# Performance work log

Hardware: AMD Instinct MI355X
Metric: run time of the kernel (lower is better)

## Reference

```python
import jax, jax.numpy as jnp
import numpy as np

DT = 1e-3   # time step (s)
DX = 10.0   # grid spacing (m)


def laplacian(u):
    # 5-point stencil with zero-Dirichlet boundaries; u: (B, ny, nx)
    up = jnp.pad(u, ((0, 0), (1, 1), (1, 1)))
    return (up[:, 2:, 1:-1] + up[:, :-2, 1:-1]
            + up[:, 1:-1, 2:] + up[:, 1:-1, :-2]
            - 4.0 * u) / (DX * DX)


def setup_inputs() -> dict:
    key = jax.random.key(0)
    ks = jax.random.split(key, 6)
    B, ny, nx, nt, R = 4, 256, 256, 300, 128
    x = jax.random.normal(ks[0], (B, nt), dtype=jnp.float32)          # source wavelets
    vp = 1500.0 + 1000.0 * jax.random.uniform(ks[1], (ny, nx), dtype=jnp.float32)
    src_y = jax.random.randint(ks[2], (B,), 2, ny - 2)
    src_x = jax.random.randint(ks[3], (B,), 2, nx - 2)
    rec_y = jax.random.randint(ks[4], (R,), 2, ny - 2)
    rec_x = jax.random.randint(ks[5], (R,), 2, nx - 2)
    return {"x": x, "vp": vp, "src_y": src_y, "src_x": src_x,
            "rec_y": rec_y, "rec_x": rec_x}


def reference(x, vp, src_y, src_x, rec_y, rec_x):
    # x: (B, nt) source amplitudes; vp: (ny, nx) velocity model.
    B = x.shape[0]
    ny, nx = vp.shape
    c2dt2 = (vp * vp) * (DT * DT)        # (ny, nx), vp^2 dt^2
    bidx = jnp.arange(B)

    def step(carry, xt):
        h1, h2 = carry                                    # u_t, u_{t-1}
        hn = 2.0 * h1 - h2 + c2dt2[None] * laplacian(h1)  # leapfrog update
        hn = hn.at[bidx, src_y, src_x].add(xt)            # source injection (scatter)
        rec = hn[:, rec_y, rec_x]                         # probe gather -> (B, R)
        return (hn, h1), rec

    h0 = jnp.zeros((B, ny, nx), dtype=x.dtype)
    _, recs = jax.lax.scan(step, (h0, h0), x.T)           # recs: (nt, B, R)
    y = jnp.transpose(recs, (0, 2, 1))                    # (nt, R, B) as in torch permute(1,2,0)
    return y
```

## Files before the change

kernel.cpp:

```cpp
#include <hip/hip_runtime.h>


constexpr int B_   = 4;
constexpr int NY   = 256;
constexpr int NX   = 256;
constexpr int NT   = 300;
constexpr int RCV  = 128;

constexpr int QB   = 16;
constexpr int RB   = NY / QB;
constexpr int W    = 8;
constexpr int EXT  = RB + 2 * W;
constexpr int GRIDB= 128;
constexpr int NTHR = 512;
constexpr int ROWS = 4;
constexpr int NW   = EXT / ROWS;
constexpr int SLABR= EXT + 2;
constexpr int PUBR = 2 * W - 1;
constexpr int LINKS= B_ * (QB - 1);
constexpr size_t HALO_FLOATS = (size_t)LINKS * 2 * 2 * PUBR * NX;
constexpr size_t HALO_BYTES  = HALO_FLOATS * sizeof(float);
constexpr int FSTR = 64;
constexpr size_t CTRL_INTS = (size_t)GRIDB * FSTR + GRIDB;
constexpr int SPIN_LIM = 1 << 20;

typedef float f32x4 __attribute__((ext_vector_type(4)));

__device__ __forceinline__ void at_store2(float* p, float a, float b) {
    float2 v = make_float2(a, b);
    unsigned long long u;
    __builtin_memcpy(&u, &v, 8);
    __hip_atomic_store((unsigned long long*)p, u, __ATOMIC_RELAXED,
                       __HIP_MEMORY_SCOPE_AGENT);
}
__device__ __forceinline__ float2 at_load2(const float* p) {
    unsigned long long u = __hip_atomic_load((const unsigned long long*)p,
                                             __ATOMIC_RELAXED,
                                             __HIP_MEMORY_SCOPE_AGENT);
    float2 v;
    __builtin_memcpy(&v, &u, 8);
    return v;
}
__device__ __forceinline__ int ld_flag_sc0(const int* p) {
    int v;
    asm volatile("global_load_dword %0, %1, off sc0\n\ts_waitcnt vmcnt(0)"
                 : "=v"(v) : "v"(p) : "memory");
    return v;
}
__device__ __forceinline__ void pub2(float* dst, const float v[4]) {
    *reinterpret_cast<float4*>(dst) = make_float4(v[0], v[1], v[2], v[3]);
    at_store2(dst, v[0], v[1]);
    at_store2(dst + 2, v[2], v[3]);
}
__device__ __forceinline__ void ing2(const float* src, float v[4], bool fast) {
    if (fast) {
        f32x4 t;
        asm volatile("global_load_dwordx4 %0, %1, off sc0\n\ts_waitcnt vmcnt(0)"
                     : "=v"(t) : "v"(src) : "memory");
        v[0] = t.x; v[1] = t.y; v[2] = t.z; v[3] = t.w;
    } else {
        float2 a = at_load2(src), b2 = at_load2(src + 2);
        v[0] = a.x; v[1] = a.y; v[2] = b2.x; v[3] = b2.y;
    }
}
__device__ __forceinline__ bool dual_wait(const int* fastp, const int* slowp,
                                          int tgt) {
    int g = 0;
    for (;;) {
        if (ld_flag_sc0(fastp) >= tgt) return true;
        if (__hip_atomic_load(slowp, __ATOMIC_RELAXED,
                              __HIP_MEMORY_SCOPE_AGENT) >= tgt) return false;
        if (++g > SPIN_LIM) return false;
        __builtin_amdgcn_s_sleep(1);
    }
}

__global__ __launch_bounds__(NTHR, 1)
void wave_df2(const float* __restrict__ x,
              const float* __restrict__ vp,
              const int*   __restrict__ src_y,
              const int*   __restrict__ src_x,
              const int*   __restrict__ rec_y,
              const int*   __restrict__ rec_x,
              float*       __restrict__ y,
              float*       __restrict__ halo,
              int*         __restrict__ ctrl)
{
    const int blk = blockIdx.x;
    const int b = blk & 7;
    if (b >= B_) return;
    const int q = blk >> 3;

    __shared__ float slabs[2][SLABR][NX];

    const int tid = threadIdx.x;
    const int r0 = q * RB;
    const int w = tid >> 6, lane = tid & 63;
    const int c0 = lane * 4;
    const int e0 = ROWS * w;

    int* fastf = ctrl;
    int* slowf = ctrl + GRIDB * FSTR;

    for (int i = tid; i < 2 * SLABR * NX; i += NTHR) ((float*)slabs)[i] = 0.f;

    const float scale = 1e-8f;
    float hA[ROWS][4], hB[ROWS][4], c2[ROWS][4];
#pragma unroll
    for (int rr = 0; rr < ROWS; ++rr) {
        const int gr = r0 - W + e0 + rr;
        if (gr >= 0 && gr < NY) {
            float4 v = *reinterpret_cast<const float4*>(&vp[gr * NX + c0]);
            c2[rr][0] = v.x * v.x * scale; c2[rr][1] = v.y * v.y * scale;
            c2[rr][2] = v.z * v.z * scale; c2[rr][3] = v.w * v.w * scale;
        } else {
#pragma unroll
            for (int j = 0; j < 4; ++j) c2[rr][j] = 0.f;
        }
#pragma unroll
        for (int j = 0; j < 4; ++j) { hA[rr][j] = 0.f; hB[rr][j] = 0.f; }
    }

    const int sy = src_y[b], sx = src_x[b];
    const int es = sy - r0 + W;
    const bool src_mine = (es >= e0) && (es < e0 + ROWS) && ((sx >> 2) == lane);
    const int s_j = sx & 3;

    bool rec_mine = false; int rec_addr = 0; float* yp = nullptr;
    if (tid < RCV) {
        const int ry = rec_y[tid], rx = rec_x[tid];
        rec_mine = (ry >= r0) && (ry < r0 + RB);
        rec_addr = (ry - r0 + W + 1) * NX + rx;
        yp = y + tid * B_ + b;
    }

    const float* xb = x + b * NT;
    const size_t lnkQ  = (size_t)(b * (QB - 1) + (q < QB - 1 ? q : 0));
    const size_t lnkQm = (size_t)(b * (QB - 1) + (q > 0 ? q - 1 : 0));
    float*       pubDn  = halo + ((lnkQ  * 2 + 0) * 2) * PUBR * NX;
    float*       pubUp  = halo + ((lnkQm * 2 + 1) * 2) * PUBR * NX;
    const float* ingTop = halo + ((lnkQm * 2 + 0) * 2) * PUBR * NX;
    const float* ingBot = halo + ((lnkQ  * 2 + 1) * 2) * PUBR * NX;

    __syncthreads();
    int exch = 0;

#define STEP(HO, HN, tt)                                                       \
    {                                                                          \
        const int cur = (tt) & 1, nxt = ((tt) + 1) & 1;                        \
        if ((tt) > 0 && rec_mine)                                              \
            yp[(size_t)((tt) - 1) * RCV * B_] =                                \
                ((const float*)slabs[cur])[rec_addr];                          \
        const float4 u4 = *reinterpret_cast<const float4*>(&slabs[cur][e0][c0]);\
        const float4 d4 = *reinterpret_cast<const float4*>(&slabs[cur][e0+ROWS+1][c0]);\
        const float ua[4] = {u4.x, u4.y, u4.z, u4.w};                          \
        const float da[4] = {d4.x, d4.y, d4.z, d4.w};                          \
        const float xt = xb[tt];                                               \
        _Pragma("unroll")                                                      \
        for (int rr = 0; rr < ROWS; ++rr) {                                    \
            float lv = __shfl_up(HO[rr][3], 1);   if (lane == 0)  lv = 0.f;    \
            float rv = __shfl_down(HO[rr][0], 1); if (lane == 63) rv = 0.f;    \
            _Pragma("unroll")                                                  \
            for (int j = 0; j < 4; ++j) {                                      \
                const float uu = (rr == 0)      ? ua[j] : HO[rr-1][j];         \
                const float dd = (rr == ROWS-1) ? da[j] : HO[rr+1][j];         \
                const float ll = (j == 0) ? lv : HO[rr][j-1];                  \
                const float rr2= (j == 3) ? rv : HO[rr][j+1];                  \
                HN[rr][j] = 2.f*HO[rr][j] - HN[rr][j]                          \
                          + c2[rr][j]*(uu + dd + ll + rr2 - 4.f*HO[rr][j]);    \
            }                                                                  \
        }                                                                      \
        if (src_mine) {                                                        \
            _Pragma("unroll")                                                  \
            for (int rr = 0; rr < ROWS; ++rr)                                  \
                _Pragma("unroll")                                              \
                for (int j = 0; j < 4; ++j)                                    \
                    if (e0 + rr == es && j == s_j) HN[rr][j] += xt;            \
        }                                                                      \
        _Pragma("unroll")                                                      \
        for (int rr = 0; rr < ROWS; ++rr)                                      \
            *reinterpret_cast<float4*>(&slabs[nxt][e0+1+rr][c0]) =             \
                make_float4(HN[rr][0], HN[rr][1], HN[rr][2], HN[rr][3]);       \
        if ((((tt) + 1) & 7) == 0) {                                           \
            ++exch;                                                            \
            const size_t soff = (size_t)(exch & 1) * PUBR * NX;                \
            _Pragma("unroll")                                                  \
            for (int rr = 0; rr < ROWS; ++rr) {                                \
                const int ext = e0 + rr;                                       \
                if (q < QB-1) {                    \
                    if (ext >= 16 && ext < 24)                                 \
                        pub2(pubDn + soff + (ext-16)*NX + c0, HN[rr]);         \
                    if (ext >= 17 && ext < 24)                                 \
                        pub2(pubDn + soff + (8+ext-17)*NX + c0, HO[rr]);       \
                }                                                              \
                if (q > 0) {                           \
                    if (ext >= 8 && ext < 16)                                  \
                        pub2(pubUp + soff + (ext-8)*NX + c0, HN[rr]);          \
                    if (ext >= 8 && ext < 15)                                  \
                        pub2(pubUp + soff + (8+ext-8)*NX + c0, HO[rr]);        \
                }                                                              \
            }                                                                  \
            __syncthreads();    \
            if (tid == 0) {                                                    \
                ((volatile int*)fastf)[blk * FSTR] = exch;        \
                __hip_atomic_store(&slowf[blk], exch, __ATOMIC_RELAXED,        \
                                   __HIP_MEMORY_SCOPE_AGENT);     \
            }                                                                  \
            if (q > 0 && w <= 1) {                   \
                const bool fast = dual_wait(&fastf[(blk-8)*FSTR],              \
                                            &slowf[blk-8], exch);              \
                _Pragma("unroll")                                              \
                for (int rr = 0; rr < ROWS; ++rr) {                            \
                    const int ext = e0 + rr;                                   \
                    if (ext < 8) {                                             \
                        ing2(ingTop + soff + ext*NX + c0, HN[rr], fast);       \
                        *reinterpret_cast<float4*>(&slabs[nxt][ext+1][c0]) =   \
                            make_float4(HN[rr][0],HN[rr][1],HN[rr][2],HN[rr][3]);\
                        if (ext >= 1)                                          \
                            ing2(ingTop + soff + (7+ext)*NX + c0, HO[rr], fast);\
                    }                                                          \
                }                                                              \
            }                                                                  \
            if (q < QB-1 && w >= NW-2) {        \
                const bool fast = dual_wait(&fastf[(blk+8)*FSTR],              \
                                            &slowf[blk+8], exch);              \
                _Pragma("unroll")                                              \
                for (int rr = 0; rr < ROWS; ++rr) {                            \
                    const int ext = e0 + rr;                                   \
                    if (ext >= 24) {                                           \
                        ing2(ingBot + soff + (ext-24)*NX + c0, HN[rr], fast);  \
                        *reinterpret_cast<float4*>(&slabs[nxt][ext+1][c0]) =   \
                            make_float4(HN[rr][0],HN[rr][1],HN[rr][2],HN[rr][3]);\
                        if (ext < 31)                                          \
                            ing2(ingBot + soff + (8+ext-24)*NX + c0, HO[rr], fast);\
                    }                                                          \
                }                                                              \
            }                                                                  \
            __syncthreads();                                                   \
        } else {                                                               \
            __syncthreads();                                                   \
        }                                                                      \
    }

    for (int t = 0; t < NT; t += 2) {
        STEP(hA, hB, t)
        STEP(hB, hA, t + 1)
    }
#undef STEP

    if (rec_mine)
        yp[(size_t)(NT - 1) * RCV * B_] = ((const float*)slabs[0])[rec_addr];
}

extern "C" void kernel_launch(void* const* d_in, const int* in_sizes, int n_in,
                              void* d_out, int out_size, void* d_ws, size_t ws_size,
                              hipStream_t stream) {
    const float* x     = (const float*)d_in[0];
    const float* vp    = (const float*)d_in[1];
    const int*   src_y = (const int*)d_in[2];
    const int*   src_x = (const int*)d_in[3];
    const int*   rec_y = (const int*)d_in[4];
    const int*   rec_x = (const int*)d_in[5];
    float*       y     = (float*)d_out;

    float* halo = (float*)d_ws;
    int*   ctrl = (int*)((char*)d_ws + HALO_BYTES);

    hipMemsetAsync(ctrl, 0, CTRL_INTS * sizeof(int), stream);

    wave_df2<<<GRIDB, NTHR, 0, stream>>>(x, vp, src_y, src_x, rec_y, rec_x,
                                         y, halo, ctrl);
}
```

Measured before the change: 371.4 us.

## Template kernel on band count, use 32 bands and LDS edge exchange

```diff
diff --git a/kernel.cpp b/kernel.cpp
--- a/kernel.cpp
+++ b/kernel.cpp
@@ -6,22 +6,11 @@
 constexpr int NX   = 256;
 constexpr int NT   = 300;
 constexpr int RCV  = 128;
-
-constexpr int QB   = 16;
-constexpr int RB   = NY / QB;
 constexpr int W    = 8;
-constexpr int EXT  = RB + 2 * W;
-constexpr int GRIDB= 128;
 constexpr int NTHR = 512;
-constexpr int ROWS = 4;
-constexpr int NW   = EXT / ROWS;
-constexpr int SLABR= EXT + 2;
 constexpr int PUBR = 2 * W - 1;
-constexpr int LINKS= B_ * (QB - 1);
-constexpr size_t HALO_FLOATS = (size_t)LINKS * 2 * 2 * PUBR * NX;
-constexpr size_t HALO_BYTES  = HALO_FLOATS * sizeof(float);
 constexpr int FSTR = 64;
-constexpr size_t CTRL_INTS = (size_t)GRIDB * FSTR + GRIDB;
+constexpr int EW   = 132;
 constexpr int SPIN_LIM = 1 << 20;
 
 typedef float f32x4 __attribute__((ext_vector_type(4)));
@@ -75,23 +64,31 @@
     }
 }
 
+template<int QB>
 __global__ __launch_bounds__(NTHR, 1)
-void wave_df2(const float* __restrict__ x,
-              const float* __restrict__ vp,
-              const int*   __restrict__ src_y,
-              const int*   __restrict__ src_x,
-              const int*   __restrict__ rec_y,
-              const int*   __restrict__ rec_x,
-              float*       __restrict__ y,
-              float*       __restrict__ halo,
-              int*         __restrict__ ctrl)
+void wave_k(const float* __restrict__ x,
+            const float* __restrict__ vp,
+            const int*   __restrict__ src_y,
+            const int*   __restrict__ src_x,
+            const int*   __restrict__ rec_y,
+            const int*   __restrict__ rec_x,
+            float*       __restrict__ y,
+            float*       __restrict__ halo,
+            int*         __restrict__ ctrl)
 {
+    constexpr int RB    = NY / QB;
+    constexpr int EXT   = RB + 2 * W;
+    constexpr int ROWS  = EXT / 8;
+    constexpr int SLABR = EXT + 2;
+    constexpr int GRIDB = 8 * QB;
+
     const int blk = blockIdx.x;
     const int b = blk & 7;
     if (b >= B_) return;
     const int q = blk >> 3;
 
     __shared__ float slabs[2][SLABR][NX];
+    __shared__ float edge[EXT][EW];
 
     const int tid = threadIdx.x;
     const int r0 = q * RB;
@@ -103,6 +100,7 @@
     int* slowf = ctrl + GRIDB * FSTR;
 
     for (int i = tid; i < 2 * SLABR * NX; i += NTHR) ((float*)slabs)[i] = 0.f;
+    for (int i = tid; i < EXT * EW; i += NTHR) ((float*)edge)[i] = 0.f;
 
     const float scale = 1e-8f;
     float hA[ROWS][4], hB[ROWS][4], c2[ROWS][4];
@@ -155,17 +153,22 @@
         const float4 d4 = *reinterpret_cast<const float4*>(&slabs[cur][e0+ROWS+1][c0]);\
         const float ua[4] = {u4.x, u4.y, u4.z, u4.w};                          \
         const float da[4] = {d4.x, d4.y, d4.z, d4.w};                          \
+        float lvv[ROWS], rvv[ROWS];                                            \
+        _Pragma("unroll")                                                      \
+        for (int rr = 0; rr < ROWS; ++rr) {     \
+            const float* er = &edge[e0 + rr][0];                               \
+            lvv[rr] = er[2 * lane];              \
+            rvv[rr] = er[2 * lane + 3];          \
+        }                                                                      \
         const float xt = xb[tt];                                               \
         _Pragma("unroll")                                                      \
         for (int rr = 0; rr < ROWS; ++rr) {                                    \
-            float lv = __shfl_up(HO[rr][3], 1);   if (lane == 0)  lv = 0.f;    \
-            float rv = __shfl_down(HO[rr][0], 1); if (lane == 63) rv = 0.f;    \
             _Pragma("unroll")                                                  \
             for (int j = 0; j < 4; ++j) {                                      \
                 const float uu = (rr == 0)      ? ua[j] : HO[rr-1][j];         \
                 const float dd = (rr == ROWS-1) ? da[j] : HO[rr+1][j];         \
-                const float ll = (j == 0) ? lv : HO[rr][j-1];                  \
-                const float rr2= (j == 3) ? rv : HO[rr][j+1];                  \
+                const float ll = (j == 0) ? lvv[rr] : HO[rr][j-1];             \
+                const float rr2= (j == 3) ? rvv[rr] : HO[rr][j+1];             \
                 HN[rr][j] = 2.f*HO[rr][j] - HN[rr][j]                          \
                           + c2[rr][j]*(uu + dd + ll + rr2 - 4.f*HO[rr][j]);    \
             }                                                                  \
@@ -178,26 +181,29 @@
                     if (e0 + rr == es && j == s_j) HN[rr][j] += xt;            \
         }                                                                      \
         _Pragma("unroll")                                                      \
-        for (int rr = 0; rr < ROWS; ++rr)                                      \
+        for (int rr = 0; rr < ROWS; ++rr) {    \
             *reinterpret_cast<float4*>(&slabs[nxt][e0+1+rr][c0]) =             \
                 make_float4(HN[rr][0], HN[rr][1], HN[rr][2], HN[rr][3]);       \
+            edge[e0 + rr][2 * lane + 1] = HN[rr][0];                           \
+            edge[e0 + rr][2 * lane + 2] = HN[rr][3];                           \
+        }                                                                      \
         if ((((tt) + 1) & 7) == 0) {                                           \
             ++exch;                                                            \
             const size_t soff = (size_t)(exch & 1) * PUBR * NX;                \
             _Pragma("unroll")                                                  \
             for (int rr = 0; rr < ROWS; ++rr) {                                \
                 const int ext = e0 + rr;                                       \
-                if (q < QB-1) {                    \
-                    if (ext >= 16 && ext < 24)                                 \
-                        pub2(pubDn + soff + (ext-16)*NX + c0, HN[rr]);         \
-                    if (ext >= 17 && ext < 24)                                 \
-                        pub2(pubDn + soff + (8+ext-17)*NX + c0, HO[rr]);       \
-                }                                                              \
-                if (q > 0) {                           \
-                    if (ext >= 8 && ext < 16)                                  \
-                        pub2(pubUp + soff + (ext-8)*NX + c0, HN[rr]);          \
-                    if (ext >= 8 && ext < 15)                                  \
-                        pub2(pubUp + soff + (8+ext-8)*NX + c0, HO[rr]);        \
+                if (q < QB-1) {                      \
+                    if (ext >= RB && ext < RB + W)                             \
+                        pub2(pubDn + soff + (ext-RB)*NX + c0, HN[rr]);         \
+                    if (ext >= RB + 1 && ext < RB + W)                         \
+                        pub2(pubDn + soff + (W+ext-RB-1)*NX + c0, HO[rr]);     \
+                }                                                              \
+                if (q > 0) {                          \
+                    if (ext >= W && ext < 2*W)                                 \
+                        pub2(pubUp + soff + (ext-W)*NX + c0, HN[rr]);          \
+                    if (ext >= W && ext < 2*W - 1)                             \
+                        pub2(pubUp + soff + (W+ext-W)*NX + c0, HO[rr]);        \
                 }                                                              \
             }                                                                  \
             __syncthreads();    \
@@ -206,33 +212,37 @@
                 __hip_atomic_store(&slowf[blk], exch, __ATOMIC_RELAXED,        \
                                    __HIP_MEMORY_SCOPE_AGENT);     \
             }                                                                  \
-            if (q > 0 && w <= 1) {                   \
+            if (q > 0 && e0 < W) {                   \
                 const bool fast = dual_wait(&fastf[(blk-8)*FSTR],              \
                                             &slowf[blk-8], exch);              \
                 _Pragma("unroll")                                              \
                 for (int rr = 0; rr < ROWS; ++rr) {                            \
                     const int ext = e0 + rr;                                   \
-                    if (ext < 8) {                                             \
+                    if (ext < W) {                                             \
                         ing2(ingTop + soff + ext*NX + c0, HN[rr], fast);       \
                         *reinterpret_cast<float4*>(&slabs[nxt][ext+1][c0]) =   \
                             make_float4(HN[rr][0],HN[rr][1],HN[rr][2],HN[rr][3]);\
+                        edge[ext][2*lane+1] = HN[rr][0];                       \
+                        edge[ext][2*lane+2] = HN[rr][3];                       \
                         if (ext >= 1)                                          \
-                            ing2(ingTop + soff + (7+ext)*NX + c0, HO[rr], fast);\
+                            ing2(ingTop + soff + (W-1+ext)*NX + c0, HO[rr], fast);\
                     }                                                          \
                 }                                                              \
             }                                                                  \
-            if (q < QB-1 && w >= NW-2) {        \
+            if (q < QB-1 && e0 + ROWS > EXT - W) {          \
                 const bool fast = dual_wait(&fastf[(blk+8)*FSTR],              \
                                             &slowf[blk+8], exch);              \
                 _Pragma("unroll")                                              \
                 for (int rr = 0; rr < ROWS; ++rr) {                            \
                     const int ext = e0 + rr;                                   \
-                    if (ext >= 24) {                                           \
-                        ing2(ingBot + soff + (ext-24)*NX + c0, HN[rr], fast);  \
+                    if (ext >= EXT - W) {                                      \
+                        ing2(ingBot + soff + (ext-(EXT-W))*NX + c0, HN[rr], fast);\
                         *reinterpret_cast<float4*>(&slabs[nxt][ext+1][c0]) =   \
                             make_float4(HN[rr][0],HN[rr][1],HN[rr][2],HN[rr][3]);\
-                        if (ext < 31)                                          \
-                            ing2(ingBot + soff + (8+ext-24)*NX + c0, HO[rr], fast);\
+                        edge[ext][2*lane+1] = HN[rr][0];                       \
+                        edge[ext][2*lane+2] = HN[rr][3];                       \
+                        if (ext < EXT - 1)                                     \
+                            ing2(ingBot + soff + (W+ext-(EXT-W))*NX + c0, HO[rr], fast);\
                     }                                                          \
                 }                                                              \
             }                                                                  \
@@ -262,12 +272,22 @@
     const int*   rec_y = (const int*)d_in[4];
     const int*   rec_x = (const int*)d_in[5];
     float*       y     = (float*)d_out;
-
-    float* halo = (float*)d_ws;
-    int*   ctrl = (int*)((char*)d_ws + HALO_BYTES);
-
-    hipMemsetAsync(ctrl, 0, CTRL_INTS * sizeof(int), stream);
-
-    wave_df2<<<GRIDB, NTHR, 0, stream>>>(x, vp, src_y, src_x, rec_y, rec_x,
-                                         y, halo, ctrl);
-}
+    float*       halo  = (float*)d_ws;
+
+    constexpr size_t HB32 = (size_t)(B_ * 31) * 2 * 2 * PUBR * NX * sizeof(float);
+    constexpr size_t CT32 = ((size_t)256 * FSTR + 256) * sizeof(int);
+    constexpr size_t HB16 = (size_t)(B_ * 15) * 2 * 2 * PUBR * NX * sizeof(float);
+    constexpr size_t CT16 = ((size_t)128 * FSTR + 128) * sizeof(int);
+
+    if (ws_size >= HB32 + CT32) {
+        int* ctrl = (int*)((char*)d_ws + HB32);
+        hipMemsetAsync(ctrl, 0, CT32, stream);
+        wave_k<32><<<256, NTHR, 0, stream>>>(x, vp, src_y, src_x, rec_y, rec_x,
+                                             y, halo, ctrl);
+    } else {
+        int* ctrl = (int*)((char*)d_ws + HB16);
+        hipMemsetAsync(ctrl, 0, CT16, stream);
+        wave_k<16><<<128, NTHR, 0, stream>>>(x, vp, src_y, src_x, rec_y, rec_x,
+                                             y, halo, ctrl);
+    }
+}
```

New measurement: 301.0 us. -18.9%, faster.
